# Optimization experiments

Measured on AMD Instinct MI355X. Metric: run time of the kernel, lower is better.

## Reference

```python
import jax, jax.numpy as jnp
import numpy as np

N_ITEMS = 50000
N_USERS = 20000
N_NODES = N_ITEMS + N_USERS
D = 128
N_REL = 3
NNZ = 800000
K_LAYERS = 2
B, S, L = 256, 4, 50


def setup_inputs() -> dict:
    key = jax.random.key(0)
    ks = iter(jax.random.split(key, 40))
    stdv = float(1.0 / np.sqrt(D))

    def uni(shape):
        return jax.random.uniform(next(ks), shape, jnp.float32, -stdv, stdv)

    id_emb = (jax.random.normal(next(ks), (N_ITEMS, D), jnp.float32) * 0.1).at[0].set(0.0)  # padding_idx=0
    user_emb = jax.random.normal(next(ks), (N_USERS, D), jnp.float32) * 0.1
    inp = dict(
        id_emb=id_emb, user_emb=user_emb,
        lin_r_w=uni((K_LAYERS, N_REL, D, D)),
        upi_w=uni((K_LAYERS, D, D)), upi_b=uni((K_LAYERS, D)),
        upu_w=uni((K_LAYERS, D, D)), upu_b=uni((K_LAYERS, D)),
        w_ih=uni((3 * D, 2 * D)), w_hh=uni((3 * D, D)),
        b_ih=uni((3 * D,)), b_hh=uni((3 * D,)),
        b_iah=uni((D,)), b_oah=uni((D,)),
        ei_w=uni((D, D)), ei_b=uni((D,)),
        eo_w=uni((D, D)), eo_b=uni((D,)),
        q1_w=uni((D, D)), q2_w=uni((D, D)), att_w=uni((D,)),
        fuse_w=uni((D, 2 * D)), fuse_b=uni((D,)),
    )
    # global heterogeneous graph: COO per relation over item+user nodes
    inp['rel_rows'] = jax.random.randint(next(ks), (N_REL, NNZ), 0, N_NODES, dtype=jnp.int32)
    inp['rel_cols'] = jax.random.randint(next(ks), (N_REL, NNZ), 0, N_NODES, dtype=jnp.int32)
    inp['rel_vals'] = jax.random.uniform(next(ks), (N_REL, NNZ), jnp.float32) * 0.1
    # session batch: every session has length in [2, L]
    lens = jax.random.randint(next(ks), (B, S), 2, L + 1)
    raw = jax.random.randint(next(ks), (B, S, L), 1, N_ITEMS)
    inp['ids'] = (raw * (jnp.arange(L)[None, None, :] < lens[:, :, None])).astype(jnp.int32)
    inp['uid'] = jax.random.randint(next(ks), (B,), 0, N_USERS, dtype=jnp.int32)
    inp['u_type'] = jax.random.randint(next(ks), (B,), 0, 3).astype(jnp.float32)
    return inp


def _hgnn(h_item, h_user, rel_rows, rel_cols, rel_vals, lin_r_w, upi_w, upi_b, upu_w, upu_b):
    Ni = h_item.shape[0]
    N = Ni + h_user.shape[0]
    for k in range(lin_r_w.shape[0]):
        h_all = jnp.concatenate([h_item, h_user], 0)
        msg = jnp.zeros_like(h_all)
        for r in range(rel_rows.shape[0]):
            Wh = h_all @ lin_r_w[k, r].T  # per-relation linear
            msg = msg + jax.ops.segment_sum(Wh[rel_cols[r]] * rel_vals[r][:, None],
                                            rel_rows[r], num_segments=N)  # sparse.mm
        h_item = jax.nn.relu((msg[:Ni] + h_item) @ upi_w[k].T + upi_b[k])
        h_user = jax.nn.relu((msg[Ni:] + h_user) @ upu_w[k].T + upu_b[k])
    return h_item, h_user


def reference(id_emb, user_emb, lin_r_w, upi_w, upi_b, upu_w, upu_b,
              w_ih, w_hh, b_ih, b_hh, b_iah, b_oah,
              ei_w, ei_b, eo_w, eo_b, q1_w, q2_w, att_w, fuse_w, fuse_b,
              rel_rows, rel_cols, rel_vals, ids, uid, u_type):
    Bb, Ss, Ll = ids.shape
    N = Ss * Bb
    ids_sb = jnp.transpose(ids, (1, 0, 2)).reshape(N, Ll)  # session-major, matches torch concat order
    lens = (ids_sb != 0).sum(-1)  # >= 2 by construction -> all sessions valid
    rows = jnp.arange(N)
    target = ids_sb[rows, lens - 1]
    Lp = Ll - 1
    m_in = jnp.arange(Lp)[None, :] < (lens - 1)[:, None]
    seq_in = ids_sb[:, :Lp] * m_in
    # session graph: consecutive-item edges; in-half sub-diagonal, out-half super-diagonal
    valid = (m_in[:, 1:] & m_in[:, :-1]).astype(jnp.float32)  # [N, Lp-1]
    i1 = jnp.arange(1, Lp)
    i0 = jnp.arange(Lp - 1)
    a_in = jnp.zeros((N, Lp, Lp), jnp.float32).at[:, i1, i0].set(valid)
    a_out = jnp.zeros((N, Lp, Lp), jnp.float32).at[:, i0, i1].set(valid)
    deg = jnp.clip(a_in.sum(-1), 1.0, None)[..., None]
    a_in = a_in / deg
    a_out = a_out / deg
    h = id_emb[seq_in]  # [N, Lp, D]
    # SessionGNN GRU-style cell (step=1)
    m_i = jnp.matmul(a_in, h @ ei_w.T + ei_b) + b_iah
    m_o = jnp.matmul(a_out, h @ eo_w.T + eo_b) + b_oah
    gi = jnp.concatenate([m_i, m_o], -1) @ w_ih.T + b_ih
    gh = h @ w_hh.T + b_hh
    i_r, i_i, i_n = jnp.split(gi, 3, -1)
    h_r, h_i, h_n = jnp.split(gh, 3, -1)
    rg = jax.nn.sigmoid(i_r + h_r)
    zg = jax.nn.sigmoid(i_i + h_i)
    ng = jnp.tanh(i_n + rg * h_n)
    h = ng + zg * (h - ng)
    # attention readout
    ht = h[rows, jnp.clip(lens - 2, 0, None)]
    alpha = jax.nn.sigmoid((ht @ q1_w.T)[:, None, :] + h @ q2_w.T) @ att_w  # [N, Lp]
    alpha = alpha * m_in.astype(jnp.float32)
    alpha = alpha / (alpha.sum(1, keepdims=True) + 1e-8)
    c_cur = jnp.einsum('nl,nld->nd', alpha, h)
    # global HGNN user context
    g_item, g_user = _hgnn(id_emb[:N_ITEMS], user_emb[:N_USERS], rel_rows, rel_cols,
                           rel_vals, lin_r_w, upi_w, upi_b, upu_w, upu_b)
    c_hist = g_user[jnp.tile(uid, Ss)]
    reps = jnp.concatenate([c_cur, c_hist], -1) @ fuse_w.T + fuse_b
    return reps, target, jnp.tile(u_type, Ss)
```

## Files before the change

kernel.cpp:

```cpp
#include <hip/hip_runtime.h>
#include <hip/hip_bf16.h>

typedef __hip_bfloat16 bf16;
typedef unsigned int uint32;
typedef __attribute__((ext_vector_type(8))) short short8;
typedef __attribute__((ext_vector_type(4))) float f32x4;

#define N_ITEMS_C 50000
#define N_USERS_C 20000
#define N_NODES_C 70000
#define NNZ_C 800000
#define NSESS 1024
#define LP 49
#define NTOK (NSESS * LP)
#define NBK 137

__device__ __forceinline__ float bflo(uint32 u) { return __uint_as_float(u << 16); }
__device__ __forceinline__ float bfhi(uint32 u) { return __uint_as_float(u & 0xffff0000u); }
__device__ __forceinline__ uint32 packbf(float a, float b) {
    return (uint32)__bfloat16_as_ushort(__float2bfloat16(a)) |
           ((uint32)__bfloat16_as_ushort(__float2bfloat16(b)) << 16);
}

__global__ void init_hab_kernel(const float2* __restrict__ idp, const float2* __restrict__ usp,
                                uint32* __restrict__ hab) {
    int i = blockIdx.x * 256 + threadIdx.x;
    float2 w = (i < 3200000) ? idp[i] : usp[i - 3200000];
    hab[i] = packbf(w.x, w.y);
}

__global__ __launch_bounds__(256) void bucket_hist_kernel(
    const int* __restrict__ rel_rows, int* __restrict__ bhist)
{
    __shared__ int hist[NBK];
    const int r = blockIdx.y, tid = threadIdx.x;
    if (tid < NBK) hist[tid] = 0;
    __syncthreads();
    const int* rr = rel_rows + (size_t)r * NNZ_C;
#pragma unroll
    for (int i = 0; i < 16; ++i) {
        int e = blockIdx.x * 4096 + i * 256 + tid;
        if (e < NNZ_C) atomicAdd(&hist[rr[e] >> 9], 1);
    }
    __syncthreads();
    if (tid < NBK && hist[tid]) atomicAdd(&bhist[r * NBK + tid], hist[tid]);
}

__global__ __launch_bounds__(256) void bucket_scan_kernel(
    const int* __restrict__ bhist, int* __restrict__ bbase)
{
    __shared__ int s[256];
    const int tid = threadIdx.x;
    for (int r = 0; r < 3; ++r) {
        s[tid] = (tid < NBK) ? bhist[r * NBK + tid] : 0;
        __syncthreads();
        for (int d = 1; d < 256; d <<= 1) {
            int t = (tid >= d) ? s[tid - d] : 0;
            __syncthreads();
            s[tid] += t;
            __syncthreads();
        }
        if (tid < NBK) bbase[r * (NBK + 1) + tid + 1] = s[tid];
        if (tid == 0) bbase[r * (NBK + 1)] = 0;
        __syncthreads();
    }
}

__global__ __launch_bounds__(256) void bucket_scatter_kernel(
    const int* __restrict__ rel_rows, const int* __restrict__ rel_cols,
    const float* __restrict__ rel_vals, const int* __restrict__ bbase,
    int* __restrict__ cursor, int2* __restrict__ tmp)
{
    __shared__ int hist[NBK], gbase[NBK], cur2[NBK];
    const int r = blockIdx.y, tid = threadIdx.x;
    if (tid < NBK) { hist[tid] = 0; cur2[tid] = 0; }
    __syncthreads();
    const int* rr = rel_rows + (size_t)r * NNZ_C;
    const int* rc = rel_cols + (size_t)r * NNZ_C;
    const float* rv = rel_vals + (size_t)r * NNZ_C;
#pragma unroll
    for (int i = 0; i < 16; ++i) {
        int e = blockIdx.x * 4096 + i * 256 + tid;
        if (e < NNZ_C) atomicAdd(&hist[rr[e] >> 9], 1);
    }
    __syncthreads();
    if (tid < NBK)
        gbase[tid] = bbase[r * (NBK + 1) + tid] +
                     (hist[tid] ? atomicAdd(&cursor[r * NBK + tid], hist[tid]) : 0);
    __syncthreads();
    int2* tp = tmp + (size_t)r * NNZ_C;
#pragma unroll
    for (int i = 0; i < 16; ++i) {
        int e = blockIdx.x * 4096 + i * 256 + tid;
        if (e < NNZ_C) {
            int row = rr[e];
            int bk = row >> 9;
            int rank = atomicAdd(&cur2[bk], 1);
            uint32 fb = __float_as_uint(rv[e]);
            uint32 pk = (uint32)rc[e] | (((fb >> 16) & 0x7FFFu) << 17);
            tp[gbase[bk] + rank] = make_int2((int)pk, row);
        }
    }
}

__global__ __launch_bounds__(256) void bucket_refine_kernel(
    const int2* __restrict__ tmp, const int* __restrict__ bbase,
    int* __restrict__ offs, uint32* __restrict__ edges)
{
    __shared__ int cnt[512], offsL[512], cur[512];
    __shared__ uint32 outb[6656];
    const int b = blockIdx.x, r = blockIdx.y, tid = threadIdx.x;
    const int lane = tid & 63, wid = tid >> 6;
    const int row0 = b << 9;
    const int e0 = bbase[r * (NBK + 1) + b];
    const int e1 = bbase[r * (NBK + 1) + b + 1];
    cnt[tid] = 0; cnt[256 + tid] = 0; cur[tid] = 0; cur[256 + tid] = 0;
    __syncthreads();
    const int2* tp = tmp + (size_t)r * NNZ_C;
    for (int e = e0 + tid; e < e1; e += 256)
        atomicAdd(&cnt[tp[e].y - row0], 1);
    __syncthreads();
    if (wid == 0) {
        int carry = 0;
        for (int c = 0; c < 8; ++c) {
            int x = cnt[c * 64 + lane];
            int inc = x;
#pragma unroll
            for (int d = 1; d < 64; d <<= 1) {
                int y = __shfl_up(inc, d, 64);
                if (lane >= d) inc += y;
            }
            offsL[c * 64 + lane] = inc - x + carry;
            carry += __shfl(inc, 63, 64);
        }
    }
    __syncthreads();
    for (int i = tid; i < 512; i += 256) {
        int row = row0 + i;
        if (row < 70001) offs[(size_t)r * 70001 + row] = e0 + offsL[i];
    }
    for (int e = e0 + tid; e < e1; e += 256) {
        int2 E = tp[e];
        int lr_ = E.y - row0;
        int slot = offsL[lr_] + atomicAdd(&cur[lr_], 1);
        if (slot < 6656) outb[slot] = (uint32)E.x;
    }
    __syncthreads();
    uint32* eo = edges + (size_t)r * NNZ_C + e0;
    for (int i = tid; i < e1 - e0; i += 256) eo[i] = outb[i];
}

__global__ __launch_bounds__(256) void gather_kernel(
    const uint32* __restrict__ hab, const uint32* __restrict__ edges,
    const int* __restrict__ offs, uint32* __restrict__ T)
{
    const int r = blockIdx.y;
    const int row = blockIdx.x * 4 + (threadIdx.x >> 6);
    const int lane = threadIdx.x & 63;
    const int grp = lane >> 4;
    const int ql  = lane & 15;
    const uint32* __restrict__ ed = edges + (size_t)r * NNZ_C;
    const int* __restrict__ of = offs + (size_t)r * 70001;
    const int e0 = of[row], e1 = of[row + 1];
    float a0 = 0.f, a1 = 0.f, a2 = 0.f, a3 = 0.f;
    float a4 = 0.f, a5 = 0.f, a6 = 0.f, a7 = 0.f;
    for (int eb = e0; eb < e1; eb += 4) {
        int eidx = eb + grp;
        bool live = eidx < e1;
        uint32 E = ed[live ? eidx : e1 - 1];
        float v = live ? __uint_as_float((E >> 1) & 0x7FFF0000u) : 0.f;
        uint4 u = *(const uint4*)&hab[(size_t)(E & 0x1FFFFu) * 64 + ql * 4];
        a0 += v * bflo(u.x); a1 += v * bfhi(u.x);
        a2 += v * bflo(u.y); a3 += v * bfhi(u.y);
        a4 += v * bflo(u.z); a5 += v * bfhi(u.z);
        a6 += v * bflo(u.w); a7 += v * bfhi(u.w);
    }
#pragma unroll
    for (int off = 16; off < 64; off <<= 1) {
        a0 += __shfl_xor(a0, off, 64); a1 += __shfl_xor(a1, off, 64);
        a2 += __shfl_xor(a2, off, 64); a3 += __shfl_xor(a3, off, 64);
        a4 += __shfl_xor(a4, off, 64); a5 += __shfl_xor(a5, off, 64);
        a6 += __shfl_xor(a6, off, 64); a7 += __shfl_xor(a7, off, 64);
    }
    if (grp == 0) {
        uint4 o;
        o.x = packbf(a0, a1); o.y = packbf(a2, a3);
        o.z = packbf(a4, a5); o.w = packbf(a6, a7);
        *(uint4*)&T[(size_t)row * 192 + r * 64 + ql * 4] = o;
    }
}

__global__ __launch_bounds__(256, 3) void wprep_kernel(
    const float* __restrict__ upi_w, const float* __restrict__ upu_w,
    const float* __restrict__ lin_r_w, int k, uint32* __restrict__ Wcat)
{
    __shared__ float As[128][65];
    __shared__ __align__(8) bf16 Ws[128][66];
    const int which = blockIdx.y, seg = which / 3, r = which % 3;
    const float* U  = (seg == 0 ? upi_w : upu_w) + (size_t)k * 16384;
    const float* Wr = lin_r_w + (size_t)(k * 3 + r) * 16384;
    uint32* out = Wcat + (size_t)seg * 32768;
    const int tid = threadIdx.x;
    const int row0 = blockIdx.x * 64;
#pragma unroll
    for (int i = 0; i < 8; ++i) {
        int id = i * 256 + tid;
        int rr = id >> 5, c4 = (id & 31) << 2;
        float4 v = *(const float4*)&U[(size_t)(row0 + rr) * 128 + c4];
        As[c4][rr] = v.x; As[c4+1][rr] = v.y; As[c4+2][rr] = v.z; As[c4+3][rr] = v.w;
    }
    const int m0 = (tid & 15) * 4;
    const int n0 = (tid >> 4) * 8;
    float acc[4][8];
#pragma unroll
    for (int i = 0; i < 4; ++i)
#pragma unroll
        for (int j = 0; j < 8; ++j) acc[i][j] = 0.f;
    for (int p = 0; p < 2; ++p) {
        if (p) __syncthreads();
        for (int i = 0; i < 32; ++i) {
            int id = i * 256 + tid;
            int c = id >> 6, kf = id & 63;
            Ws[c][kf] = __float2bfloat16(Wr[(size_t)(p * 64 + kf) * 128 + c]);
        }
        __syncthreads();
        for (int k2 = 0; k2 < 32; ++k2) {
            int kk = p * 64 + 2 * k2;
            float av0[4], av1[4];
#pragma unroll
            for (int i = 0; i < 4; ++i) { av0[i] = As[kk][m0 + i]; av1[i] = As[kk + 1][m0 + i]; }
#pragma unroll
            for (int j = 0; j < 8; ++j) {
                uint32 wp = *(const uint32*)&Ws[n0 + j][2 * k2];
                float w0 = bflo(wp), w1 = bfhi(wp);
#pragma unroll
                for (int i = 0; i < 4; ++i)
                    acc[i][j] = fmaf(av1[i], w1, fmaf(av0[i], w0, acc[i][j]));
            }
        }
    }
#pragma unroll
    for (int i = 0; i < 4; ++i) {
        int n = row0 + m0 + i;
#pragma unroll
        for (int j = 0; j < 8; j += 2)
            out[(size_t)n * 256 + (r * 128 + n0 + j) / 2] = packbf(acc[i][j], acc[i][j + 1]);
    }
}

__global__ __launch_bounds__(256) void upack_kernel(
    const float* __restrict__ upi_w, const float* __restrict__ upu_w,
    int k, uint32* __restrict__ Wcat)
{
    int id = blockIdx.x * 256 + threadIdx.x;
    int seg = id >> 13, p = id & 8191;
    int n = p >> 6, j2 = (p & 63);
    const float* U = (seg ? upu_w : upi_w) + (size_t)k * 16384;
    float2 w = *(const float2*)&U[(size_t)n * 128 + j2 * 2];
    Wcat[(size_t)seg * 32768 + (size_t)n * 256 + 192 + j2] = packbf(w.x, w.y);
}

__global__ __launch_bounds__(256) void hgnn_update_mfma_kernel(
    const bf16* __restrict__ T, uint32* __restrict__ hab,
    const bf16* __restrict__ Wcat, const float* __restrict__ bias, int row0, int M)
{
    const int tid = threadIdx.x;
    const int wv = tid >> 6, lane = tid & 63, quad = lane >> 4, lr = lane & 15;
    const int rbase = blockIdx.x * 64;
    const bf16* hb = (const bf16*)hab;
    f32x4 acc[4][2];
#pragma unroll
    for (int mt = 0; mt < 4; ++mt) { acc[mt][0] = (f32x4){0,0,0,0}; acc[mt][1] = (f32x4){0,0,0,0}; }
    int arow[4];
#pragma unroll
    for (int mt = 0; mt < 4; ++mt) {
        int rr = rbase + mt * 16 + lr;
        arow[mt] = row0 + (rr < M ? rr : M - 1);
    }
#pragma unroll
    for (int ks = 0; ks < 16; ++ks) {
        short8 b0 = *(const short8*)&Wcat[(size_t)(wv * 32 + lr) * 512 + ks * 32 + quad * 8];
        short8 b1 = *(const short8*)&Wcat[(size_t)(wv * 32 + 16 + lr) * 512 + ks * 32 + quad * 8];
#pragma unroll
        for (int mt = 0; mt < 4; ++mt) {
            short8 a;
            if (ks < 12) a = *(const short8*)&T[(size_t)arow[mt] * 384 + ks * 32 + quad * 8];
            else         a = *(const short8*)&hb[(size_t)arow[mt] * 128 + (ks - 12) * 32 + quad * 8];
            acc[mt][0] = __builtin_amdgcn_mfma_f32_16x16x32_bf16(a, b0, acc[mt][0], 0, 0, 0);
            acc[mt][1] = __builtin_amdgcn_mfma_f32_16x16x32_bf16(a, b1, acc[mt][1], 0, 0, 0);
        }
    }
    __syncthreads();
    unsigned short* hw = (unsigned short*)hab;
#pragma unroll
    for (int s = 0; s < 2; ++s) {
        int col = wv * 32 + s * 16 + lr;
        float bv = bias[col];
#pragma unroll
        for (int mt = 0; mt < 4; ++mt)
#pragma unroll
            for (int reg = 0; reg < 4; ++reg) {
                int rr = rbase + mt * 16 + quad * 4 + reg;
                if (rr < M) {
                    float v = fmaxf(acc[mt][s][reg] + bv, 0.f);
                    hw[(size_t)(row0 + rr) * 128 + col] = __bfloat16_as_ushort(__float2bfloat16(v));
                }
            }
    }
}

__global__ __launch_bounds__(256) void mfma_nt_kernel(
    const bf16* __restrict__ A, const int* __restrict__ rowmap,
    const bf16* __restrict__ W0, const bf16* __restrict__ W1,
    const float* __restrict__ b0, const float* __restrict__ b1,
    float* __restrict__ O0, float* __restrict__ O1, int M)
{
    const int tid = threadIdx.x;
    const int wv = tid >> 6, lane = tid & 63, quad = lane >> 4, lr = lane & 15;
    const int rbase = blockIdx.x * 64;
    int arow[4];
#pragma unroll
    for (int mt = 0; mt < 4; ++mt) {
        int rr = rbase + mt * 16 + lr;
        rr = rr < M ? rr : M - 1;
        arow[mt] = rowmap ? rowmap[rr] : rr;
    }
    f32x4 acc0[4][2], acc1[4][2];
#pragma unroll
    for (int mt = 0; mt < 4; ++mt) {
        acc0[mt][0] = (f32x4){0,0,0,0}; acc0[mt][1] = (f32x4){0,0,0,0};
        acc1[mt][0] = (f32x4){0,0,0,0}; acc1[mt][1] = (f32x4){0,0,0,0};
    }
#pragma unroll
    for (int ks = 0; ks < 4; ++ks) {
        short8 b00 = *(const short8*)&W0[(size_t)(wv * 32 + lr) * 128 + ks * 32 + quad * 8];
        short8 b01 = *(const short8*)&W0[(size_t)(wv * 32 + 16 + lr) * 128 + ks * 32 + quad * 8];
        short8 b10, b11;
        if (W1) {
            b10 = *(const short8*)&W1[(size_t)(wv * 32 + lr) * 128 + ks * 32 + quad * 8];
            b11 = *(const short8*)&W1[(size_t)(wv * 32 + 16 + lr) * 128 + ks * 32 + quad * 8];
        }
#pragma unroll
        for (int mt = 0; mt < 4; ++mt) {
            short8 a = *(const short8*)&A[(size_t)arow[mt] * 128 + ks * 32 + quad * 8];
            acc0[mt][0] = __builtin_amdgcn_mfma_f32_16x16x32_bf16(a, b00, acc0[mt][0], 0, 0, 0);
            acc0[mt][1] = __builtin_amdgcn_mfma_f32_16x16x32_bf16(a, b01, acc0[mt][1], 0, 0, 0);
            if (W1) {
                acc1[mt][0] = __builtin_amdgcn_mfma_f32_16x16x32_bf16(a, b10, acc1[mt][0], 0, 0, 0);
                acc1[mt][1] = __builtin_amdgcn_mfma_f32_16x16x32_bf16(a, b11, acc1[mt][1], 0, 0, 0);
            }
        }
    }
#pragma unroll
    for (int s = 0; s < 2; ++s) {
        int col = wv * 32 + s * 16 + lr;
        float bv0 = b0 ? b0[col] : 0.f;
        float bv1 = (W1 && b1) ? b1[col] : 0.f;
#pragma unroll
        for (int mt = 0; mt < 4; ++mt)
#pragma unroll
            for (int reg = 0; reg < 4; ++reg) {
                int rr = rbase + mt * 16 + quad * 4 + reg;
                if (rr < M) {
                    O0[(size_t)rr * 128 + col] = acc0[mt][s][reg] + bv0;
                    if (W1) O1[(size_t)rr * 128 + col] = acc1[mt][s][reg] + bv1;
                }
            }
    }
}

__global__ void session_prep_kernel(const int* __restrict__ ids, const int* __restrict__ uid,
                                    const float* __restrict__ u_type,
                                    int* __restrict__ lens, int* __restrict__ rowmap,
                                    float* __restrict__ out_target, float* __restrict__ out_utype)
{
    int n = blockIdx.x * 256 + threadIdx.x;
    if (n >= NSESS) return;
    int b = n & 255, s = n >> 8;
    const int* row = ids + (size_t)(b * 4 + s) * 50;
    int len = 0;
#pragma unroll
    for (int l = 0; l < 50; ++l) len += (row[l] != 0) ? 1 : 0;
    lens[n] = len;
    rowmap[n] = n * LP + (len - 2);
    out_target[n] = (float)row[len - 1];
    out_utype[n] = u_type[b];
}

__global__ void chist_kernel(const uint32* __restrict__ hab, const int* __restrict__ uid,
                             float* __restrict__ chist) {
    int n = blockIdx.x, d = threadIdx.x;
    uint32 u = hab[(size_t)(N_ITEMS_C + uid[n & 255]) * 64 + (d >> 1)];
    chist[(size_t)n * 128 + d] = (d & 1) ? bfhi(u) : bflo(u);
}

__global__ void h0_gather_kernel(const float* __restrict__ id_emb, const int* __restrict__ ids,
                                 const int* __restrict__ lens, uint32* __restrict__ hb) {
    int g = blockIdx.x, d = threadIdx.x;
    int n = g / LP;
    int tt = g - n * LP;
    int len = lens[n];
    int b = n & 255, s = n >> 8;
    int id = (tt < len - 1) ? ids[(size_t)(b * 4 + s) * 50 + tt] : 0;
    float2 e = *(const float2*)&id_emb[(size_t)id * 128 + d * 2];
    hb[(size_t)g * 64 + d] = packbf(e.x, e.y);
}

__global__ __launch_bounds__(256) void epack_kernel(
    const float* __restrict__ w_ih, const float* __restrict__ w_hh,
    const float* __restrict__ ei_w, const float* __restrict__ eo_w,
    const float* __restrict__ q2_w, const float* __restrict__ q1_w,
    uint32* __restrict__ dst)
{
    int id = blockIdx.x * 256 + threadIdx.x;
    const float* src; int off;
    if      (id <  49152) { src = w_ih; off = id; }
    else if (id <  73728) { src = w_hh; off = id - 49152; }
    else if (id <  81920) { src = ei_w; off = id - 73728; }
    else if (id <  90112) { src = eo_w; off = id - 81920; }
    else if (id <  98304) { src = q2_w; off = id - 90112; }
    else                  { src = q1_w; off = id - 98304; }
    float2 w = *(const float2*)&src[(size_t)off * 2];
    dst[id] = packbf(w.x, w.y);
}

__global__ __launch_bounds__(256, 2) void gru_mfma_kernel(
    const float* __restrict__ hEi, const float* __restrict__ hEo,
    uint32* __restrict__ hb, const int* __restrict__ lens,
    const bf16* __restrict__ wihb,
    const bf16* __restrict__ whhb,
    const float* __restrict__ b_ih, const float* __restrict__ b_hh,
    const float* __restrict__ b_iah, const float* __restrict__ b_oah)
{
    __shared__ __align__(16) bf16 Agi[64][264];
    __shared__ __align__(16) bf16 Agh[64][136];
    const int tid = threadIdx.x;
    const int g0 = blockIdx.x * 64;

#pragma unroll 4
    for (int i = 0; i < 32; ++i) {
        int p = i * 256 + tid;
        int row = p >> 7, kp = p & 127;
        int g = g0 + row;
        int n = g / LP;
        int tt = g - n * LP;
        int len = lens[n];
        int kk = (kp & 63) * 2;
        float v0, v1;
        if (kp < 64) {
            v0 = b_iah[kk]; v1 = b_iah[kk + 1];
            if (tt >= 1 && tt < len - 1) {
                float2 e = *(const float2*)&hEi[(size_t)(g - 1) * 128 + kk];
                v0 += e.x; v1 += e.y;
            }
        } else {
            v0 = b_oah[kk]; v1 = b_oah[kk + 1];
            if (tt < len - 2) {
                float2 e = *(const float2*)&hEo[(size_t)(g + 1) * 128 + kk];
                v0 += e.x; v1 += e.y;
            }
        }
        *(uint32*)&Agi[row][kp * 2] = packbf(v0, v1);
    }
#pragma unroll 4
    for (int i = 0; i < 16; ++i) {
        int p = i * 256 + tid;
        int row = p >> 6, kp = p & 63;
        *(uint32*)&Agh[row][kp * 2] = hb[(size_t)(g0 + row) * 64 + kp];
    }
    __syncthreads();

    const int wv = tid >> 6;
    const int lane = tid & 63;
    const int quad = lane >> 4;
    const int lr = lane & 15;
    const int c0 = wv * 32;

    f32x4 acc[4][2][4];
#pragma unroll
    for (int mt = 0; mt < 4; ++mt)
#pragma unroll
        for (int s = 0; s < 2; ++s)
#pragma unroll
            for (int j = 0; j < 4; ++j) acc[mt][s][j] = (f32x4){0.f, 0.f, 0.f, 0.f};

#pragma unroll 2
    for (int ks = 0; ks < 8; ++ks) {
        short8 bfr[2][3];
#pragma unroll
        for (int s = 0; s < 2; ++s)
#pragma unroll
            for (int gte = 0; gte < 3; ++gte) {
                int n0 = gte * 128 + c0 + s * 16 + lr;
                bfr[s][gte] = *(const short8*)&wihb[(size_t)n0 * 256 + ks * 32 + quad * 8];
            }
#pragma unroll
        for (int mt = 0; mt < 4; ++mt) {
            short8 a = *(const short8*)&Agi[mt * 16 + lr][ks * 32 + quad * 8];
#pragma unroll
            for (int s = 0; s < 2; ++s) {
                acc[mt][s][0] = __builtin_amdgcn_mfma_f32_16x16x32_bf16(a, bfr[s][0], acc[mt][s][0], 0, 0, 0);
                acc[mt][s][1] = __builtin_amdgcn_mfma_f32_16x16x32_bf16(a, bfr[s][1], acc[mt][s][1], 0, 0, 0);
                acc[mt][s][2] = __builtin_amdgcn_mfma_f32_16x16x32_bf16(a, bfr[s][2], acc[mt][s][2], 0, 0, 0);
            }
        }
    }
#pragma unroll 2
    for (int ks = 0; ks < 4; ++ks) {
        short8 bfr[2][3];
#pragma unroll
        for (int s = 0; s < 2; ++s)
#pragma unroll
            for (int gte = 0; gte < 3; ++gte) {
                int n0 = gte * 128 + c0 + s * 16 + lr;
                bfr[s][gte] = *(const short8*)&whhb[(size_t)n0 * 128 + ks * 32 + quad * 8];
            }
#pragma unroll
        for (int mt = 0; mt < 4; ++mt) {
            short8 a = *(const short8*)&Agh[mt * 16 + lr][ks * 32 + quad * 8];
#pragma unroll
            for (int s = 0; s < 2; ++s) {
                acc[mt][s][0] = __builtin_amdgcn_mfma_f32_16x16x32_bf16(a, bfr[s][0], acc[mt][s][0], 0, 0, 0);
                acc[mt][s][1] = __builtin_amdgcn_mfma_f32_16x16x32_bf16(a, bfr[s][1], acc[mt][s][1], 0, 0, 0);
                acc[mt][s][3] = __builtin_amdgcn_mfma_f32_16x16x32_bf16(a, bfr[s][2], acc[mt][s][3], 0, 0, 0);
            }
        }
    }

    unsigned short* hu = (unsigned short*)hb;
#pragma unroll
    for (int s = 0; s < 2; ++s) {
        int col = c0 + s * 16 + lr;
        float brz = b_ih[col] + b_hh[col];
        float bzz = b_ih[col + 128] + b_hh[col + 128];
        float bin = b_ih[col + 256];
        float bhn = b_hh[col + 256];
#pragma unroll
        for (int mt = 0; mt < 4; ++mt)
#pragma unroll
            for (int reg = 0; reg < 4; ++reg) {
                int row = g0 + mt * 16 + quad * 4 + reg;
                float rg = 1.f / (1.f + expf(-(acc[mt][s][0][reg] + brz)));
                float zg = 1.f / (1.f + expf(-(acc[mt][s][1][reg] + bzz)));
                float ng = tanhf(acc[mt][s][2][reg] + bin + rg * (acc[mt][s][3][reg] + bhn));
                size_t idx = (size_t)row * 128 + col;
                float ho = __uint_as_float((uint32)hu[idx] << 16);
                hu[idx] = __bfloat16_as_ushort(__float2bfloat16(ng + zg * (ho - ng)));
            }
    }
}

__global__ __launch_bounds__(128) void attn_fuse_kernel(
    const float* __restrict__ q1h, const float* __restrict__ q2h,
    const unsigned short* __restrict__ hu, const float* __restrict__ chist,
    const int* __restrict__ lens, const float* __restrict__ att_w,
    const float* __restrict__ fuse_w, const float* __restrict__ fuse_b,
    float* __restrict__ out)
{
    __shared__ float q1s[128], aws[128], al[64], cv[256];
    const int n = blockIdx.x, tid = threadIdx.x;
    q1s[tid] = q1h[(size_t)n * 128 + tid];
    aws[tid] = att_w[tid];
    if (tid < 64) al[tid] = 0.f;
    __syncthreads();
    const int len = lens[n];
    if (tid < len - 1) {
        const float* q2 = &q2h[(size_t)(n * LP + tid) * 128];
        float s = 0.f;
        for (int d = 0; d < 128; ++d) {
            float x = q1s[d] + q2[d];
            s += aws[d] / (1.f + expf(-x));
        }
        al[tid] = s;
    }
    __syncthreads();
    float ssum = 0.f;
    for (int t = 0; t < len - 1; ++t) ssum += al[t];
    float inv = 1.f / (ssum + 1e-8f);
    float c = 0.f;
    for (int t = 0; t < len - 1; ++t) {
        float hv = __uint_as_float((uint32)hu[(size_t)(n * LP + t) * 128 + tid] << 16);
        c += al[t] * inv * hv;
    }
    cv[tid] = c;
    cv[128 + tid] = chist[(size_t)n * 128 + tid];
    __syncthreads();
    float s = fuse_b[tid];
    const float* fr = fuse_w + (size_t)tid * 256;
    for (int k = 0; k < 256; ++k) s += cv[k] * fr[k];
    out[(size_t)n * 128 + tid] = s;
}

extern "C" void kernel_launch(void* const* d_in, const int* in_sizes, int n_in,
                              void* d_out, int out_size, void* d_ws, size_t ws_size,
                              hipStream_t stream)
{
    const float* id_emb   = (const float*)d_in[0];
    const float* user_emb = (const float*)d_in[1];
    const float* lin_r_w  = (const float*)d_in[2];
    const float* upi_w    = (const float*)d_in[3];
    const float* upi_b    = (const float*)d_in[4];
    const float* upu_w    = (const float*)d_in[5];
    const float* upu_b    = (const float*)d_in[6];
    const float* w_ih     = (const float*)d_in[7];
    const float* w_hh     = (const float*)d_in[8];
    const float* b_ih     = (const float*)d_in[9];
    const float* b_hh     = (const float*)d_in[10];
    const float* b_iah    = (const float*)d_in[11];
    const float* b_oah    = (const float*)d_in[12];
    const float* ei_w     = (const float*)d_in[13];
    const float* ei_b     = (const float*)d_in[14];
    const float* eo_w     = (const float*)d_in[15];
    const float* eo_b     = (const float*)d_in[16];
    const float* q1_w     = (const float*)d_in[17];
    const float* q2_w     = (const float*)d_in[18];
    const float* att_w    = (const float*)d_in[19];
    const float* fuse_w   = (const float*)d_in[20];
    const float* fuse_b   = (const float*)d_in[21];
    const int*  rel_rows  = (const int*)d_in[22];
    const int*  rel_cols  = (const int*)d_in[23];
    const float* rel_vals = (const float*)d_in[24];
    const int*  ids       = (const int*)d_in[25];
    const int*  uid       = (const int*)d_in[26];
    const float* u_type   = (const float*)d_in[27];
    float* out = (float*)d_out;

    uint32* W32    = (uint32*)d_ws;
    uint32* hab    = W32;
    uint32* T      = W32 + 4480000;
    uint32* edges  = W32 + 17920000;
    int2*   tmp    = (int2*)(W32 + 20320000);
    int*    offs   = (int*)(W32 + 25120000);
    int*    bhist  = (int*)(W32 + 25330004);
    int*    cursor = (int*)(W32 + 25330415);
    int*    bbase  = (int*)(W32 + 25330826);
    uint32* Wcat   = W32 + 25331240;
    float*  q1h    = (float*)(W32 + 25396776);
    float*  chist  = (float*)(W32 + 25527848);
    int*    lens   = (int*)(W32 + 25658920);
    int*    rowmap = (int*)(W32 + 25659944);
    uint32* sess_hb = W32;
    float* sess_Ei  = (float*)(W32 + 4480000);
    float* sess_Eo  = (float*)(W32 + 10902528);
    float* q2h      = sess_Ei;
    uint32* wpk     = W32 + 17920000;
    uint32* wihb = wpk;
    uint32* whhb = wpk + 49152;
    uint32* eiwb = wpk + 73728;
    uint32* eowb = wpk + 81920;
    uint32* q2wb = wpk + 90112;
    uint32* q1wb = wpk + 98304;
    if (ws_size < (size_t)27144192 * 4 + 4096) return;

    init_hab_kernel<<<17500, 256, 0, stream>>>((const float2*)id_emb, (const float2*)user_emb, hab);
    hipMemsetAsync(bhist, 0, (size_t)822 * 4, stream);
    bucket_hist_kernel<<<dim3(196, 3), 256, 0, stream>>>(rel_rows, bhist);
    bucket_scan_kernel<<<1, 256, 0, stream>>>(bhist, bbase);
    bucket_scatter_kernel<<<dim3(196, 3), 256, 0, stream>>>(rel_rows, rel_cols, rel_vals,
                                                            bbase, cursor, tmp);
    bucket_refine_kernel<<<dim3(NBK, 3), 256, 0, stream>>>(tmp, bbase, offs, edges);

    for (int k = 0; k < 2; ++k) {
        wprep_kernel<<<dim3(2, 6), 256, 0, stream>>>(upi_w, upu_w, lin_r_w, k, Wcat);
        upack_kernel<<<64, 256, 0, stream>>>(upi_w, upu_w, k, Wcat);
        gather_kernel<<<dim3(17500, 3), 256, 0, stream>>>(hab, edges, offs, T);
        hgnn_update_mfma_kernel<<<782, 256, 0, stream>>>((const bf16*)T, hab,
            (const bf16*)Wcat, upi_b + k * 128, 0, N_ITEMS_C);
        hgnn_update_mfma_kernel<<<313, 256, 0, stream>>>((const bf16*)T, hab,
            (const bf16*)(Wcat + 32768), upu_b + k * 128, N_ITEMS_C, N_USERS_C);
    }

    session_prep_kernel<<<4, 256, 0, stream>>>(ids, uid, u_type, lens, rowmap,
        out + 131072, out + 132096);
    chist_kernel<<<NSESS, 128, 0, stream>>>(hab, uid, chist);
    epack_kernel<<<416, 256, 0, stream>>>(w_ih, w_hh, ei_w, eo_w, q2_w, q1_w, wpk);
    h0_gather_kernel<<<NTOK, 64, 0, stream>>>(id_emb, ids, lens, sess_hb);
    mfma_nt_kernel<<<784, 256, 0, stream>>>((const bf16*)sess_hb, nullptr,
        (const bf16*)eiwb, (const bf16*)eowb, ei_b, eo_b, sess_Ei, sess_Eo, NTOK);
    gru_mfma_kernel<<<NTOK / 64, 256, 0, stream>>>(sess_Ei, sess_Eo, sess_hb, lens,
        (const bf16*)wihb, (const bf16*)whhb, b_ih, b_hh, b_iah, b_oah);
    mfma_nt_kernel<<<784, 256, 0, stream>>>((const bf16*)sess_hb, nullptr,
        (const bf16*)q2wb, nullptr, nullptr, nullptr, q2h, nullptr, NTOK);
    mfma_nt_kernel<<<16, 256, 0, stream>>>((const bf16*)sess_hb, rowmap,
        (const bf16*)q1wb, nullptr, nullptr, nullptr, q1h, nullptr, NSESS);
    attn_fuse_kernel<<<NSESS, 128, 0, stream>>>(q1h, q2h, (const unsigned short*)sess_hb,
        chist, lens, att_w, fuse_w, fuse_b, out);
}
```

Before: 809.8 us.

## Merge per-relation gather launches into one kernel with software-prefetched edge loads

The SpMM gather kernel now loops over all three relations inside one wave per row instead of launching a separate grid dimension per relation. Each relation loop software-pipelines the next edge index and embedding row load ahead of the current FMA, and accumulation uses packed float2 vectors. The aim is to hide gather latency and cut the number of blocks launched. In exchange, each wave holds more registers (24 accumulators plus prefetched data), parallelism per launch drops threefold, and reductions are batched.

After: 776.8 us. -4.1%, faster.

```diff
diff --git a/kernel.cpp b/kernel.cpp
--- a/kernel.cpp
+++ b/kernel.cpp
@@ -5,6 +5,7 @@
 typedef unsigned int uint32;
 typedef __attribute__((ext_vector_type(8))) short short8;
 typedef __attribute__((ext_vector_type(4))) float f32x4;
+typedef __attribute__((ext_vector_type(2))) float f32x2;
 
 #define N_ITEMS_C 50000
 #define N_USERS_C 20000
@@ -154,39 +155,54 @@
     const uint32* __restrict__ hab, const uint32* __restrict__ edges,
     const int* __restrict__ offs, uint32* __restrict__ T)
 {
-    const int r = blockIdx.y;
     const int row = blockIdx.x * 4 + (threadIdx.x >> 6);
     const int lane = threadIdx.x & 63;
     const int grp = lane >> 4;
     const int ql  = lane & 15;
-    const uint32* __restrict__ ed = edges + (size_t)r * NNZ_C;
-    const int* __restrict__ of = offs + (size_t)r * 70001;
-    const int e0 = of[row], e1 = of[row + 1];
-    float a0 = 0.f, a1 = 0.f, a2 = 0.f, a3 = 0.f;
-    float a4 = 0.f, a5 = 0.f, a6 = 0.f, a7 = 0.f;
-    for (int eb = e0; eb < e1; eb += 4) {
-        int eidx = eb + grp;
-        bool live = eidx < e1;
-        uint32 E = ed[live ? eidx : e1 - 1];
-        float v = live ? __uint_as_float((E >> 1) & 0x7FFF0000u) : 0.f;
-        uint4 u = *(const uint4*)&hab[(size_t)(E & 0x1FFFFu) * 64 + ql * 4];
-        a0 += v * bflo(u.x); a1 += v * bfhi(u.x);
-        a2 += v * bflo(u.y); a3 += v * bfhi(u.y);
-        a4 += v * bflo(u.z); a5 += v * bfhi(u.z);
-        a6 += v * bflo(u.w); a7 += v * bfhi(u.w);
-    }
-#pragma unroll
-    for (int off = 16; off < 64; off <<= 1) {
-        a0 += __shfl_xor(a0, off, 64); a1 += __shfl_xor(a1, off, 64);
-        a2 += __shfl_xor(a2, off, 64); a3 += __shfl_xor(a3, off, 64);
-        a4 += __shfl_xor(a4, off, 64); a5 += __shfl_xor(a5, off, 64);
-        a6 += __shfl_xor(a6, off, 64); a7 += __shfl_xor(a7, off, 64);
-    }
+    const uint32* __restrict__ habq = hab + ql * 4;
+    f32x2 acc[3][4];
+#pragma unroll
+    for (int r = 0; r < 3; ++r)
+#pragma unroll
+        for (int j = 0; j < 4; ++j) acc[r][j] = (f32x2){0.f, 0.f};
+#pragma unroll
+    for (int r = 0; r < 3; ++r) {
+        const uint32* __restrict__ ed = edges + (size_t)r * NNZ_C;
+        const int* __restrict__ of = offs + (size_t)r * 70001;
+        const int e0 = of[row], e1 = of[row + 1];
+        if (e0 >= e1) continue;
+        int eidx = e0 + grp;
+        uint32 E = ed[min(eidx, e1 - 1)];
+        uint4 u = *(const uint4*)&habq[(size_t)(E & 0x1FFFFu) * 64];
+        float v = (eidx < e1) ? __uint_as_float((E >> 1) & 0x7FFF0000u) : 0.f;
+        for (int eb = e0; eb < e1; eb += 4) {
+            int ein = eb + 4 + grp;
+            uint32 En = ed[min(ein, e1 - 1)];
+            uint4 un = *(const uint4*)&habq[(size_t)(En & 0x1FFFFu) * 64];
+            float vn = (ein < e1) ? __uint_as_float((En >> 1) & 0x7FFF0000u) : 0.f;
+            f32x2 vv = {v, v};
+            acc[r][0] += vv * (f32x2){bflo(u.x), bfhi(u.x)};
+            acc[r][1] += vv * (f32x2){bflo(u.y), bfhi(u.y)};
+            acc[r][2] += vv * (f32x2){bflo(u.z), bfhi(u.z)};
+            acc[r][3] += vv * (f32x2){bflo(u.w), bfhi(u.w)};
+            E = En; u = un; v = vn;
+        }
+    }
+    float* af = (float*)acc;
+#pragma unroll
+    for (int off = 16; off < 64; off <<= 1)
+#pragma unroll
+        for (int j = 0; j < 24; ++j) af[j] += __shfl_xor(af[j], off, 64);
     if (grp == 0) {
-        uint4 o;
-        o.x = packbf(a0, a1); o.y = packbf(a2, a3);
-        o.z = packbf(a4, a5); o.w = packbf(a6, a7);
-        *(uint4*)&T[(size_t)row * 192 + r * 64 + ql * 4] = o;
+#pragma unroll
+        for (int r = 0; r < 3; ++r) {
+            uint4 o;
+            o.x = packbf(acc[r][0].x, acc[r][0].y);
+            o.y = packbf(acc[r][1].x, acc[r][1].y);
+            o.z = packbf(acc[r][2].x, acc[r][2].y);
+            o.w = packbf(acc[r][3].x, acc[r][3].y);
+            *(uint4*)&T[(size_t)row * 192 + r * 64 + ql * 4] = o;
+        }
     }
 }
 
@@ -663,7 +679,7 @@
     for (int k = 0; k < 2; ++k) {
         wprep_kernel<<<dim3(2, 6), 256, 0, stream>>>(upi_w, upu_w, lin_r_w, k, Wcat);
         upack_kernel<<<64, 256, 0, stream>>>(upi_w, upu_w, k, Wcat);
-        gather_kernel<<<dim3(17500, 3), 256, 0, stream>>>(hab, edges, offs, T);
+        gather_kernel<<<17500, 256, 0, stream>>>(hab, edges, offs, T);
         hgnn_update_mfma_kernel<<<782, 256, 0, stream>>>((const bf16*)T, hab,
             (const bf16*)Wcat, upi_b + k * 128, 0, N_ITEMS_C);
         hgnn_update_mfma_kernel<<<313, 256, 0, stream>>>((const bf16*)T, hab,
```
